# Optimization experiments

Measured on AMD Instinct MI355X. Metric: run time of the kernel, lower is better.

The kernel has to match this reference:

```python
import jax, jax.numpy as jnp
import numpy as np

N_NODES = 50000
N_EDGES = 640000
D = 128
BN_EPS = 1e-5


def setup_inputs() -> dict:
    key = jax.random.key(0)
    k1, k2, k3 = jax.random.split(key, 3)
    x = jax.random.normal(k1, (N_NODES, D), dtype=jnp.float32)
    # Glorot-ish weight for GCNConv linear
    W = jax.random.normal(k2, (D, D), dtype=jnp.float32) * (1.0 / np.sqrt(D))
    b = jnp.zeros((D,), dtype=jnp.float32)
    gamma = jnp.ones((D,), dtype=jnp.float32)
    beta = jnp.zeros((D,), dtype=jnp.float32)
    edge_index = jax.random.randint(k3, (2, N_EDGES), 0, N_NODES, dtype=jnp.int64)
    return {"x": x, "W": W, "b": b, "gamma": gamma, "beta": beta, "edge_index": edge_index}


def reference(x, W, b, gamma, beta, edge_index):
    N = x.shape[0]
    # --- GCNConv: x' = D^{-1/2} (A + I) D^{-1/2} (x W) + b ---
    xw = x @ W  # [N, D]
    loops = jnp.arange(N, dtype=edge_index.dtype)
    src = jnp.concatenate([edge_index[0], loops])  # [E+N]
    dst = jnp.concatenate([edge_index[1], loops])
    ones = jnp.ones(src.shape[0], dtype=x.dtype)
    deg = jax.ops.segment_sum(ones, dst, num_segments=N)  # in-degree incl. self-loop
    dinv = jnp.where(deg > 0, jax.lax.rsqrt(deg), 0.0)
    norm = dinv[src] * dinv[dst]  # [E+N]
    msg = xw[src] * norm[:, None]  # [E+N, D] gathered + scaled messages
    h = jax.ops.segment_sum(msg, dst, num_segments=N) + b  # scatter-add aggregation
    # --- BatchNorm1d (training-mode batch stats over nodes, biased var) ---
    mean = jnp.mean(h, axis=0)
    var = jnp.mean(jnp.square(h - mean), axis=0)
    h = (h - mean) * jax.lax.rsqrt(var + BN_EPS) * gamma + beta
    # --- activation (relu) ---
    h = jax.nn.relu(h)
    # --- residual (in_channels == out_channels) ---
    h = x + h
    # --- dropout: identity in eval mode for deterministic reference ---
    return h
```

## Files before the change

### kernel.cpp

```cpp
#include <hip/hip_runtime.h>

#define DCH 128
#define ROWS 16
#define BN_EPS 1e-5f

typedef unsigned short u16;
typedef __attribute__((ext_vector_type(8))) short short8;
typedef __attribute__((ext_vector_type(4))) float floatx4;

__device__ __forceinline__ float bf2f(u16 u) {
    return __uint_as_float(((unsigned)u) << 16);
}
__device__ __forceinline__ u16 f2bf(float f) {
    unsigned u = __float_as_uint(f);
    u += 0x7FFFu + ((u >> 16) & 1u);
    return (u16)(u >> 16);
}
__device__ __forceinline__ float ldf(const void* p, int i, int isbf) {
    return isbf ? bf2f(((const u16*)p)[i]) : ((const float*)p)[i];
}

__global__ void prep_kernel(const int* ei, int ewords, const u16* xw, int* ws_i,
                            const void* W, u16* Wb, float* zbase, int zn) {
    int t = threadIdx.x;
    if (blockIdx.x == 0) {
        __shared__ int s_nz, s_hits;
        if (t == 0) { s_nz = 0; s_hits = 0; }
        __syncthreads();
        int nz = 0;
        for (int i = t; i < 1024; i += 256) {
            int w = 2 * i + 1;
            if (w < ewords) nz |= ei[w];
        }
        if (nz) atomicOr(&s_nz, 1);
        unsigned m = (xw[2 * t] >> 8) & 0x7F;
        if (m >= 0x3B && m <= 0x43) atomicAdd(&s_hits, 1);
        __syncthreads();
        int isbf = (s_hits >= 128) ? 1 : 0;
        if (t == 0) {
            ws_i[0] = (s_nz == 0) ? 1 : 0;
            ws_i[1] = isbf;
            ws_i[2] = 0;
        }
        for (int idx = t; idx < DCH * DCH; idx += 256) {
            int j = idx & 7, lane = (idx >> 3) & 63, kk = (idx >> 9) & 3, nt = idx >> 11;
            int k = kk * 32 + (lane >> 4) * 8 + j;
            int n = nt * 16 + (lane & 15);
            Wb[idx] = f2bf(ldf(W, k * DCH + n, isbf));
        }
    } else {
        int stride = (gridDim.x - 1) * 256;
        for (int i = (blockIdx.x - 1) * 256 + t; i < zn; i += stride) zbase[i] = 0.f;
    }
}

__global__ void zero_kernel(float* p, int n) {
    int stride = gridDim.x * 256;
    for (int i = blockIdx.x * 256 + threadIdx.x; i < n; i += stride) p[i] = 0.f;
}

__global__ void paint_kernel(u16* out, int n, unsigned val) {
    int stride = gridDim.x * 256;
    for (int i = blockIdx.x * 256 + threadIdx.x; i < n; i += stride) out[i] = (u16)val;
}

__global__ void detect_kernel(const int* ei, int ewords, const u16* xw, int* ws_i) {
    __shared__ int s_nz, s_hits;
    int t = threadIdx.x;
    if (t == 0) { s_nz = 0; s_hits = 0; }
    __syncthreads();
    int nz = 0;
    for (int i = t; i < 1024; i += 256) {
        int w = 2 * i + 1;
        if (w < ewords) nz |= ei[w];
    }
    if (nz) atomicOr(&s_nz, 1);
    unsigned m = (xw[2 * t] >> 8) & 0x7F;
    if (m >= 0x3B && m <= 0x43) atomicAdd(&s_hits, 1);
    __syncthreads();
    if (t == 0) {
        ws_i[0] = (s_nz == 0) ? 1 : 0;
        ws_i[1] = (s_hits >= 128) ? 1 : 0;
        ws_i[2] = 0;
    }
}

__global__ void deg_kernel(const int* ei, int E, int* ws_i, int* deg, int N) {
    int is64 = ws_i[0];
    int i = blockIdx.x * 256 + threadIdx.x;
    if (i < E) {
        int s = is64 ? ei[2 * i] : ei[i];
        int d = is64 ? ei[2 * E + 2 * i] : ei[E + i];
        if (((unsigned)s >= (unsigned)N) || ((unsigned)d >= (unsigned)N))
            atomicOr(&ws_i[2], 2);
        d = min(max(d, 0), N - 1);
        atomicAdd(&deg[d], 1);
    }
}

__global__ void dinv_kernel(const int* deg, float* dinv, int N, int* ws_i) {
    int i = blockIdx.x * 256 + threadIdx.x;
    if (i < N) {
        float v = rsqrtf((float)(deg[i] + 1));
        if (!(v > 0.f && v <= 1.001f)) atomicOr(&ws_i[2], 4);
        dinv[i] = v;
    }
}

__global__ void scanA_kernel(const int* deg, int* part, int N) {
    int base = blockIdx.x * 1024 + threadIdx.x * 4;
    int s = 0;
    #pragma unroll
    for (int j = 0; j < 4; ++j) {
        int i = base + j;
        if (i < N) s += deg[i];
    }
    #pragma unroll
    for (int o = 1; o < 64; o <<= 1) s += __shfl_xor(s, o, 64);
    __shared__ int ws4[4];
    if ((threadIdx.x & 63) == 0) ws4[threadIdx.x >> 6] = s;
    __syncthreads();
    if (threadIdx.x == 0) part[blockIdx.x] = ws4[0] + ws4[1] + ws4[2] + ws4[3];
}

__global__ void scanB_kernel(int* part, int P) {
    __shared__ int wsum[4];
    int t = threadIdx.x, lane = t & 63, w = t >> 6;
    int v = (t < P) ? part[t] : 0;
    int sc = v;
    #pragma unroll
    for (int o = 1; o < 64; o <<= 1) {
        int u = __shfl_up(sc, o, 64);
        if (lane >= o) sc += u;
    }
    if (lane == 63) wsum[w] = sc;
    __syncthreads();
    if (t < 4) {
        int s = wsum[t];
        #pragma unroll
        for (int o = 1; o < 4; o <<= 1) {
            int u = __shfl_up(s, o, 4);
            if (t >= o) s += u;
        }
        wsum[t] = s;
    }
    __syncthreads();
    int excl = sc - v + (w ? wsum[w - 1] : 0);
    if (t < P) part[t] = excl;
}

__global__ void scanC_kernel(int* deg_cursor, const int* part, int* rowptr,
                             float* dinv, int N) {
    __shared__ int wsum[4];
    int t = threadIdx.x, lane = t & 63, w = t >> 6;
    int base = blockIdx.x * 1024 + t * 4;
    int v[4], ts = 0;
    #pragma unroll
    for (int j = 0; j < 4; ++j) {
        int i = base + j;
        v[j] = (i < N) ? deg_cursor[i] : 0;
        ts += v[j];
    }
    int sc = ts;
    #pragma unroll
    for (int o = 1; o < 64; o <<= 1) {
        int u = __shfl_up(sc, o, 64);
        if (lane >= o) sc += u;
    }
    if (lane == 63) wsum[w] = sc;
    __syncthreads();
    if (t < 4) {
        int s = wsum[t];
        #pragma unroll
        for (int o = 1; o < 4; o <<= 1) {
            int u = __shfl_up(s, o, 4);
            if (t >= o) s += u;
        }
        wsum[t] = s;
    }
    __syncthreads();
    int run = sc - ts + (w ? wsum[w - 1] : 0) + part[blockIdx.x];
    #pragma unroll
    for (int j = 0; j < 4; ++j) {
        int i = base + j;
        if (i < N) {
            deg_cursor[i] = run;
            run += v[j];
            rowptr[i + 1] = run;
            dinv[i] = rsqrtf((float)(v[j] + 1));
        }
    }
    if (blockIdx.x == 0 && t == 0) rowptr[0] = 0;
}

__global__ void fillcsr_kernel(const int* ei, int E, const int* ws_i,
                               int* cursor, int* col, int N) {
    int is64 = ws_i[0];
    int i = blockIdx.x * 256 + threadIdx.x;
    if (i < E) {
        int s = is64 ? ei[2 * i] : ei[i];
        int d = is64 ? ei[2 * E + 2 * i] : ei[E + i];
        s = min(max(s, 0), N - 1);
        d = min(max(d, 0), N - 1);
        int pos = atomicAdd(&cursor[d], 1);
        col[pos] = s;
    }
}

__global__ void gemm_mfma_kernel(const void* x, const u16* Wb, const float* dinv,
                                 const int* ws_i, u16* y, int N) {
    int isbf = ws_i[1];
    int t = threadIdx.x;
    int wv = t >> 6, lane = t & 63;
    int quad = lane >> 4, l16 = lane & 15;
    int r0 = blockIdx.x * 64 + wv * 16;
    int rl = min(r0 + l16, N - 1);
    short8 a[4];
    if (isbf) {
        const u16* xp = (const u16*)x + (size_t)rl * DCH + quad * 8;
        #pragma unroll
        for (int kk = 0; kk < 4; ++kk)
            a[kk] = *(const short8*)(xp + kk * 32);
    } else {
        const float* xp = (const float*)x + (size_t)rl * DCH + quad * 8;
        #pragma unroll
        for (int kk = 0; kk < 4; ++kk) {
            float4 f0 = *(const float4*)(xp + kk * 32);
            float4 f1 = *(const float4*)(xp + kk * 32 + 4);
            short8 aa;
            aa[0] = (short)f2bf(f0.x); aa[1] = (short)f2bf(f0.y);
            aa[2] = (short)f2bf(f0.z); aa[3] = (short)f2bf(f0.w);
            aa[4] = (short)f2bf(f1.x); aa[5] = (short)f2bf(f1.y);
            aa[6] = (short)f2bf(f1.z); aa[7] = (short)f2bf(f1.w);
            a[kk] = aa;
        }
    }
    floatx4 acc[8];
    #pragma unroll
    for (int i = 0; i < 8; ++i) acc[i] = (floatx4)(0.f);
    #pragma unroll
    for (int nt = 0; nt < 8; ++nt) {
        #pragma unroll
        for (int kk = 0; kk < 4; ++kk) {
            short8 bfr = *(const short8*)&Wb[(((nt << 2) | kk) * 64 + lane) * 8];
            acc[nt] = __builtin_amdgcn_mfma_f32_16x16x32_bf16(a[kk], bfr, acc[nt], 0, 0, 0);
        }
    }
    #pragma unroll
    for (int i = 0; i < 4; ++i) {
        int row = r0 + quad * 4 + i;
        if (row < N) {
            float dv = dinv[row];
            #pragma unroll
            for (int nt = 0; nt < 8; ++nt)
                y[(size_t)row * DCH + nt * 16 + l16] = f2bf(acc[nt][i] * dv);
        }
    }
}

__global__ void gather_stats_kernel(const int* rowptr, const int* col, const u16* y,
                                    const float* dinv, const void* b, const int* ws_i,
                                    float* h, float* sums, float* sumsq, int N) {
    int isbf = ws_i[1];
    int t = threadIdx.x;
    int hw = t >> 5;
    int l32 = t & 31;
    int c0 = l32 * 4;
    float bb[4];
    #pragma unroll
    for (int k = 0; k < 4; ++k) bb[k] = ldf(b, c0 + k, isbf);
    float ps[4] = {0.f, 0.f, 0.f, 0.f}, pq[4] = {0.f, 0.f, 0.f, 0.f};
    int stream_id = blockIdx.x * 8 + hw;
    int nstreams = gridDim.x * 8;
    for (int n = stream_id; n < N; n += nstreams) {
        uint2 qs = *(const uint2*)&y[(size_t)n * DCH + c0];
        float a0[4] = { bf2f((u16)(qs.x & 0xFFFF)), bf2f((u16)(qs.x >> 16)),
                        bf2f((u16)(qs.y & 0xFFFF)), bf2f((u16)(qs.y >> 16)) };
        float a1[4] = {0.f, 0.f, 0.f, 0.f};
        float a2[4] = {0.f, 0.f, 0.f, 0.f};
        float a3[4] = {0.f, 0.f, 0.f, 0.f};
        int beg = rowptr[n], end = rowptr[n + 1];
        int j = beg;
        for (; j + 3 < end; j += 4) {
            int s0 = col[j], s1 = col[j + 1], s2 = col[j + 2], s3 = col[j + 3];
            uint2 q0 = *(const uint2*)&y[(size_t)s0 * DCH + c0];
            uint2 q1 = *(const uint2*)&y[(size_t)s1 * DCH + c0];
            uint2 q2 = *(const uint2*)&y[(size_t)s2 * DCH + c0];
            uint2 q3 = *(const uint2*)&y[(size_t)s3 * DCH + c0];
            a0[0] += bf2f((u16)(q0.x & 0xFFFF)); a0[1] += bf2f((u16)(q0.x >> 16));
            a0[2] += bf2f((u16)(q0.y & 0xFFFF)); a0[3] += bf2f((u16)(q0.y >> 16));
            a1[0] += bf2f((u16)(q1.x & 0xFFFF)); a1[1] += bf2f((u16)(q1.x >> 16));
            a1[2] += bf2f((u16)(q1.y & 0xFFFF)); a1[3] += bf2f((u16)(q1.y >> 16));
            a2[0] += bf2f((u16)(q2.x & 0xFFFF)); a2[1] += bf2f((u16)(q2.x >> 16));
            a2[2] += bf2f((u16)(q2.y & 0xFFFF)); a2[3] += bf2f((u16)(q2.y >> 16));
            a3[0] += bf2f((u16)(q3.x & 0xFFFF)); a3[1] += bf2f((u16)(q3.x >> 16));
            a3[2] += bf2f((u16)(q3.y & 0xFFFF)); a3[3] += bf2f((u16)(q3.y >> 16));
        }
        for (; j < end; ++j) {
            uint2 q0 = *(const uint2*)&y[(size_t)col[j] * DCH + c0];
            a0[0] += bf2f((u16)(q0.x & 0xFFFF)); a0[1] += bf2f((u16)(q0.x >> 16));
            a0[2] += bf2f((u16)(q0.y & 0xFFFF)); a0[3] += bf2f((u16)(q0.y >> 16));
        }
        float dn = dinv[n];
        float4 o;
        o.x = fmaf((a0[0] + a1[0]) + (a2[0] + a3[0]), dn, bb[0]);
        o.y = fmaf((a0[1] + a1[1]) + (a2[1] + a3[1]), dn, bb[1]);
        o.z = fmaf((a0[2] + a1[2]) + (a2[2] + a3[2]), dn, bb[2]);
        o.w = fmaf((a0[3] + a1[3]) + (a2[3] + a3[3]), dn, bb[3]);
        *(float4*)&h[(size_t)n * DCH + c0] = o;
        ps[0] += o.x; pq[0] += o.x * o.x;
        ps[1] += o.y; pq[1] += o.y * o.y;
        ps[2] += o.z; pq[2] += o.z * o.z;
        ps[3] += o.w; pq[3] += o.w * o.w;
    }
    __shared__ float lps[8][DCH], lpq[8][DCH];
    #pragma unroll
    for (int k = 0; k < 4; ++k) { lps[hw][c0 + k] = ps[k]; lpq[hw][c0 + k] = pq[k]; }
    __syncthreads();
    if (t < DCH) {
        int ch = (t + blockIdx.x * 16) & 127;
        float s = 0.f, q = 0.f;
        #pragma unroll
        for (int i = 0; i < 8; ++i) { s += lps[i][ch]; q += lpq[i][ch]; }
        atomicAdd(&sums[ch], s);
        atomicAdd(&sumsq[ch], q);
    }
}

__global__ void gemm_valu_kernel(const void* x, const void* W, const float* dinv,
                                 const int* ws_i, void* y, int N) {
    __shared__ float WsF[64 * DCH];
    __shared__ float xs[ROWS * DCH];
    int isbf = ws_i[1];
    int t = threadIdx.x;
    int r0 = blockIdx.x * ROWS;
    for (int i = t; i < ROWS * DCH; i += 256) {
        int r = r0 + (i >> 7);
        xs[i] = (r < N) ? ldf(x, r * DCH + (i & 127), isbf) : 0.f;
    }
    int d = t & 127, rh = t >> 7;
    float s[8];
    #pragma unroll
    for (int j = 0; j < 8; ++j) s[j] = 0.f;
    for (int half = 0; half < 2; ++half) {
        __syncthreads();
        for (int i = t; i < 64 * DCH; i += 256)
            WsF[i] = ldf(W, half * 64 * DCH + i, isbf);
        __syncthreads();
        #pragma unroll
        for (int j = 0; j < 8; ++j) {
            int rr = rh + 2 * j;
            float a = s[j];
            #pragma unroll 16
            for (int k = 0; k < 64; ++k)
                a = fmaf(xs[rr * DCH + half * 64 + k], WsF[k * DCH + d], a);
            s[j] = a;
        }
    }
    #pragma unroll
    for (int j = 0; j < 8; ++j) {
        int r = r0 + rh + 2 * j;
        if (r < N) {
            float v = s[j] * dinv[r];
            if (isbf) ((u16*)y)[r * DCH + d] = f2bf(v);
            else      ((float*)y)[r * DCH + d] = v;
        }
    }
}

__global__ void scatter_kernel(const int* ei, int E, const int* ws_i,
                               const void* y, float* acc, int N) {
    int is64 = ws_i[0], isbf = ws_i[1];
    int gid = blockIdx.x * 256 + threadIdx.x;
    int e = gid >> 5;
    if (e >= E) return;
    int c0 = (gid & 31) * 4;
    int s = is64 ? ei[2 * e] : ei[e];
    int d = is64 ? ei[2 * E + 2 * e] : ei[E + e];
    s = min(max(s, 0), N - 1);
    d = min(max(d, 0), N - 1);
    float v0, v1, v2, v3;
    if (isbf) {
        uint2 raw = *(const uint2*)&((const u16*)y)[s * DCH + c0];
        v0 = bf2f((u16)(raw.x & 0xFFFF)); v1 = bf2f((u16)(raw.x >> 16));
        v2 = bf2f((u16)(raw.y & 0xFFFF)); v3 = bf2f((u16)(raw.y >> 16));
    } else {
        float4 raw = *(const float4*)&((const float*)y)[s * DCH + c0];
        v0 = raw.x; v1 = raw.y; v2 = raw.z; v3 = raw.w;
    }
    float* a = &acc[d * DCH + c0];
    atomicAdd(a + 0, v0);
    atomicAdd(a + 1, v1);
    atomicAdd(a + 2, v2);
    atomicAdd(a + 3, v3);
}

__global__ void bnstat_kernel(const void* y, float* acc, const float* dinv,
                              const void* b, int* ws_i,
                              float* sums, float* sumsq, int total) {
    int isbf = ws_i[1];
    int t = threadIdx.x;
    int d = t & 127;
    float bb = ldf(b, d, isbf);
    float ps = 0.f, pq = 0.f;
    int stride = gridDim.x * 256;
    for (int i = blockIdx.x * 256 + t; i < total; i += stride) {
        int r = i >> 7;
        float yv = isbf ? bf2f(((const u16*)y)[i]) : ((const float*)y)[i];
        float v = (yv + acc[i]) * dinv[r] + bb;
        acc[i] = v;
        ps += v;
        pq += v * v;
    }
    __shared__ float ls[256], lq[256];
    ls[t] = ps; lq[t] = pq;
    __syncthreads();
    if (t < 128) {
        atomicAdd(&sums[d], ls[t] + ls[t + 128]);
        atomicAdd(&sumsq[d], lq[t] + lq[t + 128]);
    }
}

__global__ void out_kernel(const float* h, const void* x,
                           const void* gamma, const void* beta,
                           int* ws_i, const float* sums, const float* sumsq,
                           void* out, int total, float invN) {
    __shared__ float sc[DCH], sh[DCH];
    int isbf = ws_i[1];
    int t = threadIdx.x;
    if (t < DCH) {
        float mean = sums[t] * invN;
        float var = fmaxf(sumsq[t] * invN - mean * mean, 0.f);
        float s = ldf(gamma, t, isbf) * rsqrtf(var + BN_EPS);
        if (!(var < 1e8f && fabsf(s) < 1e6f)) atomicOr(&ws_i[2], 32);
        sc[t] = s;
        sh[t] = ldf(beta, t, isbf) - mean * s;
    }
    __syncthreads();
    int stride = gridDim.x * 256;
    if (isbf) {
        for (int i = blockIdx.x * 256 + t; i < total; i += stride) {
            int d = i & 127;
            float v = fmaf(h[i], sc[d], sh[d]);
            v = fmaxf(v, 0.f) + bf2f(((const u16*)x)[i]);
            ((u16*)out)[i] = f2bf(v);
        }
    } else {
        for (int i = blockIdx.x * 256 + t; i < total; i += stride) {
            int d = i & 127;
            float v = fmaf(h[i], sc[d], sh[d]);
            v = fmaxf(v, 0.f) + ((const float*)x)[i];
            ((float*)out)[i] = v;
        }
    }
}

__global__ void diag_kernel(const int* ws_i, void* out, int n) {
    int e = ws_i[2];
    if (!e) return;
    int isbf = ws_i[1];
    float v = 4096.f + 32.f * (float)(e & 63);
    int stride = gridDim.x * 256;
    if (isbf) {
        u16 code = f2bf(v);
        for (int i = blockIdx.x * 256 + threadIdx.x; i < n; i += stride)
            ((u16*)out)[i] = code;
    } else {
        for (int i = blockIdx.x * 256 + threadIdx.x; i < n; i += stride)
            ((float*)out)[i] = v;
    }
}

extern "C" void kernel_launch(void* const* d_in, const int* in_sizes, int n_in,
                              void* d_out, int out_size, void* d_ws, size_t ws_size,
                              hipStream_t stream) {
    const void* x     = d_in[0];
    const void* W     = d_in[1];
    const void* b     = d_in[2];
    const void* gamma = d_in[3];
    const void* beta  = d_in[4];
    const int*  ei    = (const int*)d_in[5];

    const int N  = in_sizes[0] / DCH;
    const int E  = in_sizes[5] / 2;
    const int ND = N * DCH;
    const int P  = (N + 1023) / 1024;

    char* wsb = (char*)d_ws;
    int*  ws_i = (int*)wsb;

    size_t o_wb   = 64;
    size_t o_deg  = o_wb + 32768;
    size_t o_sum  = o_deg + 4 * (size_t)N;
    size_t o_sq   = o_sum + 512;
    size_t o_rp   = o_sq + 512;
    size_t o_dinv = o_rp + 4 * ((size_t)N + 1) + 4;
    size_t o_part = o_dinv + 4 * (size_t)N;
    size_t o_h    = (o_part + 1024 + 255) & ~(size_t)255;
    size_t o_col  = o_h + 4 * (size_t)ND;
    size_t need_csr = o_col + 4 * (size_t)E;

    (void)hipGetLastError();

    if (ws_size >= need_csr) {
        u16*   Wb    = (u16*)(wsb + o_wb);
        int*   deg   = (int*)(wsb + o_deg);
        float* sums  = (float*)(wsb + o_sum);
        float* sumsq = (float*)(wsb + o_sq);
        int*   rowptr= (int*)(wsb + o_rp);
        float* dinv  = (float*)(wsb + o_dinv);
        int*   part  = (int*)(wsb + o_part);
        float* h     = (float*)(wsb + o_h);
        int*   col   = (int*)(wsb + o_col);
        u16*   y     = (u16*)d_out;

        prep_kernel<<<65, 256, 0, stream>>>(ei, 2 * E, (const u16*)x, ws_i,
                                            W, Wb, (float*)(wsb + o_deg), N + 256);
        deg_kernel<<<(E + 255) / 256, 256, 0, stream>>>(ei, E, ws_i, deg, N);
        scanA_kernel<<<P, 256, 0, stream>>>(deg, part, N);
        scanB_kernel<<<1, 256, 0, stream>>>(part, P);
        scanC_kernel<<<P, 256, 0, stream>>>(deg, part, rowptr, dinv, N);
        fillcsr_kernel<<<(E + 255) / 256, 256, 0, stream>>>(ei, E, ws_i, deg, col, N);
        gemm_mfma_kernel<<<(N + 63) / 64, 256, 0, stream>>>(x, Wb, dinv, ws_i, y, N);
        gather_stats_kernel<<<1024, 256, 0, stream>>>(rowptr, col, y, dinv, b, ws_i,
                                                      h, sums, sumsq, N);
        out_kernel<<<1024, 256, 0, stream>>>(h, x, gamma, beta, ws_i, sums, sumsq,
                                             d_out, ND, 1.0f / (float)N);
        diag_kernel<<<512, 256, 0, stream>>>(ws_i, d_out, out_size);
    } else {
        int*   deg   = (int*)(wsb + 16);
        float* dinv  = (float*)(wsb + 16 + 4 * (size_t)N);
        float* sums  = (float*)(wsb + 16 + 8 * (size_t)N);
        float* sumsq = sums + DCH;
        float* acc   = sumsq + DCH;
        size_t need = 16 + 8 * (size_t)N + 1024 + 4 * (size_t)ND;
        if (ws_size < need) {
            int mb = (int)(ws_size >> 20); if (mb > 127) mb = 127;
            float v = 2048.f + 16.f * (float)mb;
            unsigned u; __builtin_memcpy(&u, &v, 4);
            paint_kernel<<<1024, 256, 0, stream>>>((u16*)d_out, out_size, u >> 16);
            return;
        }
        detect_kernel<<<1, 256, 0, stream>>>(ei, 2 * E, (const u16*)x, ws_i);
        zero_kernel<<<2048, 256, 0, stream>>>((float*)(wsb + 16), 2 * N + 256 + ND);
        deg_kernel<<<(E + 255) / 256, 256, 0, stream>>>(ei, E, ws_i, deg, N);
        dinv_kernel<<<(N + 255) / 256, 256, 0, stream>>>(deg, dinv, N, ws_i);
        gemm_valu_kernel<<<(N + ROWS - 1) / ROWS, 256, 0, stream>>>(x, W, dinv, ws_i, d_out, N);
        scatter_kernel<<<(E * 32 + 255) / 256, 256, 0, stream>>>(ei, E, ws_i, d_out, acc, N);
        bnstat_kernel<<<240, 256, 0, stream>>>(d_out, acc, dinv, b, ws_i, sums, sumsq, ND);
        out_kernel<<<256, 256, 0, stream>>>(acc, x, gamma, beta, ws_i, sums, sumsq,
                                            d_out, ND, 1.0f / (float)N);
        diag_kernel<<<512, 256, 0, stream>>>(ws_i, d_out, out_size);
    }

    if (hipGetLastError() != hipSuccess)
        hipMemsetAsync(d_out, 0x42, (size_t)out_size * 2, stream);
}
```

Before: 250.5 us.

## Prefetch CSR indices in gather, vectorize output pass, spread W prep across blocks

The gather/stats kernel now loads the next node's rowptr, self row and next group of column indices before processing the current ones, so the dependent index loads overlap with feature gathers. It also gains launch bounds and a doubled grid. The output kernel processes four channels per thread with float4/uint2 loads and stores, with per-thread scale and shift hoisted out of the loop. The prep kernel spreads W conversion and workspace zeroing across all blocks, each block redundantly recomputing the dtype detection. The costs are more register pressure and redundant detection work.

```diff
diff --git a/kernel.cpp b/kernel.cpp
--- a/kernel.cpp
+++ b/kernel.cpp
@@ -23,35 +23,34 @@
 __global__ void prep_kernel(const int* ei, int ewords, const u16* xw, int* ws_i,
                             const void* W, u16* Wb, float* zbase, int zn) {
     int t = threadIdx.x;
+    __shared__ int s_nz, s_hits;
+    if (t == 0) { s_nz = 0; s_hits = 0; }
+    __syncthreads();
     if (blockIdx.x == 0) {
-        __shared__ int s_nz, s_hits;
-        if (t == 0) { s_nz = 0; s_hits = 0; }
-        __syncthreads();
         int nz = 0;
         for (int i = t; i < 1024; i += 256) {
             int w = 2 * i + 1;
             if (w < ewords) nz |= ei[w];
         }
         if (nz) atomicOr(&s_nz, 1);
-        unsigned m = (xw[2 * t] >> 8) & 0x7F;
-        if (m >= 0x3B && m <= 0x43) atomicAdd(&s_hits, 1);
-        __syncthreads();
-        int isbf = (s_hits >= 128) ? 1 : 0;
-        if (t == 0) {
-            ws_i[0] = (s_nz == 0) ? 1 : 0;
-            ws_i[1] = isbf;
-            ws_i[2] = 0;
-        }
-        for (int idx = t; idx < DCH * DCH; idx += 256) {
-            int j = idx & 7, lane = (idx >> 3) & 63, kk = (idx >> 9) & 3, nt = idx >> 11;
-            int k = kk * 32 + (lane >> 4) * 8 + j;
-            int n = nt * 16 + (lane & 15);
-            Wb[idx] = f2bf(ldf(W, k * DCH + n, isbf));
-        }
-    } else {
-        int stride = (gridDim.x - 1) * 256;
-        for (int i = (blockIdx.x - 1) * 256 + t; i < zn; i += stride) zbase[i] = 0.f;
-    }
+    }
+    unsigned m = (xw[2 * t] >> 8) & 0x7F;
+    if (m >= 0x3B && m <= 0x43) atomicAdd(&s_hits, 1);
+    __syncthreads();
+    int isbf = (s_hits >= 128) ? 1 : 0;
+    if (blockIdx.x == 0 && t == 0) {
+        ws_i[0] = (s_nz == 0) ? 1 : 0;
+        ws_i[1] = isbf;
+        ws_i[2] = 0;
+    }
+    int gstride = gridDim.x * 256;
+    for (int idx = blockIdx.x * 256 + t; idx < DCH * DCH; idx += gstride) {
+        int j = idx & 7, lane = (idx >> 3) & 63, kk = (idx >> 9) & 3, nt = idx >> 11;
+        int k = kk * 32 + (lane >> 4) * 8 + j;
+        int n = nt * 16 + (lane & 15);
+        Wb[idx] = f2bf(ldf(W, k * DCH + n, isbf));
+    }
+    for (int i = blockIdx.x * 256 + t; i < zn; i += gstride) zbase[i] = 0.f;
 }
 
 __global__ void zero_kernel(float* p, int n) {
@@ -258,9 +257,10 @@
     }
 }
 
-__global__ void gather_stats_kernel(const int* rowptr, const int* col, const u16* y,
-                                    const float* dinv, const void* b, const int* ws_i,
-                                    float* h, float* sums, float* sumsq, int N) {
+__global__ __launch_bounds__(256, 8)
+void gather_stats_kernel(const int* rowptr, const int* col, const u16* y,
+                         const float* dinv, const void* b, const int* ws_i,
+                         float* h, float* sums, float* sumsq, int N) {
     int isbf = ws_i[1];
     int t = threadIdx.x;
     int hw = t >> 5;
@@ -272,21 +272,42 @@
     float ps[4] = {0.f, 0.f, 0.f, 0.f}, pq[4] = {0.f, 0.f, 0.f, 0.f};
     int stream_id = blockIdx.x * 8 + hw;
     int nstreams = gridDim.x * 8;
-    for (int n = stream_id; n < N; n += nstreams) {
-        uint2 qs = *(const uint2*)&y[(size_t)n * DCH + c0];
+
+    int n = stream_id;
+    int beg = 0, end = 0;
+    uint2 qs = {0u, 0u};
+    if (n < N) {
+        beg = rowptr[n];
+        end = rowptr[n + 1];
+        qs = *(const uint2*)&y[(size_t)n * DCH + c0];
+    }
+    while (n < N) {
+        int n2 = n + nstreams;
+        int begN = 0, endN = 0;
+        uint2 qsN = {0u, 0u};
+        if (n2 < N) {
+            begN = rowptr[n2];
+            endN = rowptr[n2 + 1];
+            qsN = *(const uint2*)&y[(size_t)n2 * DCH + c0];
+        }
+
         float a0[4] = { bf2f((u16)(qs.x & 0xFFFF)), bf2f((u16)(qs.x >> 16)),
                         bf2f((u16)(qs.y & 0xFFFF)), bf2f((u16)(qs.y >> 16)) };
         float a1[4] = {0.f, 0.f, 0.f, 0.f};
         float a2[4] = {0.f, 0.f, 0.f, 0.f};
         float a3[4] = {0.f, 0.f, 0.f, 0.f};
-        int beg = rowptr[n], end = rowptr[n + 1];
         int j = beg;
-        for (; j + 3 < end; j += 4) {
-            int s0 = col[j], s1 = col[j + 1], s2 = col[j + 2], s3 = col[j + 3];
+        int s0 = 0, s1 = 0, s2 = 0, s3 = 0;
+        bool have = (j + 3 < end);
+        if (have) { s0 = col[j]; s1 = col[j + 1]; s2 = col[j + 2]; s3 = col[j + 3]; }
+        while (have) {
             uint2 q0 = *(const uint2*)&y[(size_t)s0 * DCH + c0];
             uint2 q1 = *(const uint2*)&y[(size_t)s1 * DCH + c0];
             uint2 q2 = *(const uint2*)&y[(size_t)s2 * DCH + c0];
             uint2 q3 = *(const uint2*)&y[(size_t)s3 * DCH + c0];
+            int jn = j + 4;
+            bool haven = (jn + 3 < end);
+            if (haven) { s0 = col[jn]; s1 = col[jn + 1]; s2 = col[jn + 2]; s3 = col[jn + 3]; }
             a0[0] += bf2f((u16)(q0.x & 0xFFFF)); a0[1] += bf2f((u16)(q0.x >> 16));
             a0[2] += bf2f((u16)(q0.y & 0xFFFF)); a0[3] += bf2f((u16)(q0.y >> 16));
             a1[0] += bf2f((u16)(q1.x & 0xFFFF)); a1[1] += bf2f((u16)(q1.x >> 16));
@@ -295,6 +316,7 @@
             a2[2] += bf2f((u16)(q2.y & 0xFFFF)); a2[3] += bf2f((u16)(q2.y >> 16));
             a3[0] += bf2f((u16)(q3.x & 0xFFFF)); a3[1] += bf2f((u16)(q3.x >> 16));
             a3[2] += bf2f((u16)(q3.y & 0xFFFF)); a3[3] += bf2f((u16)(q3.y >> 16));
+            j = jn; have = haven;
         }
         for (; j < end; ++j) {
             uint2 q0 = *(const uint2*)&y[(size_t)col[j] * DCH + c0];
@@ -312,6 +334,8 @@
         ps[1] += o.y; pq[1] += o.y * o.y;
         ps[2] += o.z; pq[2] += o.z * o.z;
         ps[3] += o.w; pq[3] += o.w * o.w;
+
+        n = n2; beg = begN; end = endN; qs = qsN;
     }
     __shared__ float lps[8][DCH], lpq[8][DCH];
     #pragma unroll
@@ -437,21 +461,42 @@
         sh[t] = ldf(beta, t, isbf) - mean * s;
     }
     __syncthreads();
+    int total4 = total >> 2;
     int stride = gridDim.x * 256;
+    int i0 = blockIdx.x * 256 + t;
+    int d0 = (i0 << 2) & 127;
+    float c0 = sc[d0], c1 = sc[d0 + 1], c2 = sc[d0 + 2], c3 = sc[d0 + 3];
+    float f0 = sh[d0], f1 = sh[d0 + 1], f2 = sh[d0 + 2], f3 = sh[d0 + 3];
     if (isbf) {
-        for (int i = blockIdx.x * 256 + t; i < total; i += stride) {
-            int d = i & 127;
-            float v = fmaf(h[i], sc[d], sh[d]);
-            v = fmaxf(v, 0.f) + bf2f(((const u16*)x)[i]);
-            ((u16*)out)[i] = f2bf(v);
+        for (int i = i0; i < total4; i += stride) {
+            float4 hv = ((const float4*)h)[i];
+            uint2 xv = ((const uint2*)x)[i];
+            float v0 = fmaxf(fmaf(hv.x, c0, f0), 0.f) + bf2f((u16)(xv.x & 0xFFFF));
+            float v1 = fmaxf(fmaf(hv.y, c1, f1), 0.f) + bf2f((u16)(xv.x >> 16));
+            float v2 = fmaxf(fmaf(hv.z, c2, f2), 0.f) + bf2f((u16)(xv.y & 0xFFFF));
+            float v3 = fmaxf(fmaf(hv.w, c3, f3), 0.f) + bf2f((u16)(xv.y >> 16));
+            uint2 o;
+            o.x = (unsigned)f2bf(v0) | ((unsigned)f2bf(v1) << 16);
+            o.y = (unsigned)f2bf(v2) | ((unsigned)f2bf(v3) << 16);
+            ((uint2*)out)[i] = o;
         }
     } else {
-        for (int i = blockIdx.x * 256 + t; i < total; i += stride) {
-            int d = i & 127;
-            float v = fmaf(h[i], sc[d], sh[d]);
-            v = fmaxf(v, 0.f) + ((const float*)x)[i];
-            ((float*)out)[i] = v;
-        }
+        for (int i = i0; i < total4; i += stride) {
+            float4 hv = ((const float4*)h)[i];
+            float4 xv = ((const float4*)x)[i];
+            float4 o;
+            o.x = fmaxf(fmaf(hv.x, c0, f0), 0.f) + xv.x;
+            o.y = fmaxf(fmaf(hv.y, c1, f1), 0.f) + xv.y;
+            o.z = fmaxf(fmaf(hv.z, c2, f2), 0.f) + xv.z;
+            o.w = fmaxf(fmaf(hv.w, c3, f3), 0.f) + xv.w;
+            ((float4*)out)[i] = o;
+        }
+    }
+    for (int i = (total4 << 2) + i0; i < total; i += stride) {
+        int d = i & 127;
+        float v = fmaxf(fmaf(h[i], sc[d], sh[d]), 0.f);
+        if (isbf) ((u16*)out)[i] = f2bf(v + bf2f(((const u16*)x)[i]));
+        else      ((float*)out)[i] = v + ((const float*)x)[i];
     }
 }
 
@@ -514,17 +559,17 @@
         int*   col   = (int*)(wsb + o_col);
         u16*   y     = (u16*)d_out;
 
-        prep_kernel<<<65, 256, 0, stream>>>(ei, 2 * E, (const u16*)x, ws_i,
-                                            W, Wb, (float*)(wsb + o_deg), N + 256);
+        prep_kernel<<<128, 256, 0, stream>>>(ei, 2 * E, (const u16*)x, ws_i,
+                                             W, Wb, (float*)(wsb + o_deg), N + 256);
         deg_kernel<<<(E + 255) / 256, 256, 0, stream>>>(ei, E, ws_i, deg, N);
         scanA_kernel<<<P, 256, 0, stream>>>(deg, part, N);
         scanB_kernel<<<1, 256, 0, stream>>>(part, P);
         scanC_kernel<<<P, 256, 0, stream>>>(deg, part, rowptr, dinv, N);
         fillcsr_kernel<<<(E + 255) / 256, 256, 0, stream>>>(ei, E, ws_i, deg, col, N);
         gemm_mfma_kernel<<<(N + 63) / 64, 256, 0, stream>>>(x, Wb, dinv, ws_i, y, N);
-        gather_stats_kernel<<<1024, 256, 0, stream>>>(rowptr, col, y, dinv, b, ws_i,
+        gather_stats_kernel<<<2048, 256, 0, stream>>>(rowptr, col, y, dinv, b, ws_i,
                                                       h, sums, sumsq, N);
-        out_kernel<<<1024, 256, 0, stream>>>(h, x, gamma, beta, ws_i, sums, sumsq,
+        out_kernel<<<2048, 256, 0, stream>>>(h, x, gamma, beta, ws_i, sums, sumsq,
                                              d_out, ND, 1.0f / (float)N);
         diag_kernel<<<512, 256, 0, stream>>>(ws_i, d_out, out_size);
     } else {
```

Measured after the change: 258.5 us. +3.2%, slower.
